# Performance work log

Hardware: AMD Instinct MI355X
Metric: run time of the kernel (lower is better)

Reference implementation:

```python
import jax, jax.numpy as jnp
import numpy as np

N = 50000          # nodes
E = 800000         # edges (avg degree 16)
IN_C = 3
HEADS = 4
NUM_GRAPHS = 8
NUM_CLASSES = 10


def setup_inputs() -> dict:
    key = jax.random.key(0)
    ks = jax.random.split(key, 12)
    x = jax.random.normal(ks[0], (N, IN_C), jnp.float32)
    edge_index = jax.random.randint(ks[1], (2, E), 0, N, dtype=jnp.int64)
    batch = jnp.sort(jax.random.randint(ks[2], (N,), 0, NUM_GRAPHS, dtype=jnp.int64))

    def glorot(k, shape, fan):
        return jax.random.normal(k, shape, jnp.float32) * np.float32(1.0 / np.sqrt(fan))

    return {
        "x": x, "edge_index": edge_index, "batch": batch,
        "fc0_w": glorot(ks[3], (IN_C, 16), IN_C), "fc0_b": jnp.zeros((16,), jnp.float32),
        "u1": glorot(ks[4], (16, HEADS), 16), "c1": jnp.zeros((HEADS,), jnp.float32),
        "w1": glorot(ks[5], (16, HEADS * 32), 16), "b1": jnp.zeros((32,), jnp.float32),
        "u2": glorot(ks[6], (32, HEADS), 32), "c2": jnp.zeros((HEADS,), jnp.float32),
        "w2": glorot(ks[7], (32, HEADS * 64), 32), "b2": jnp.zeros((64,), jnp.float32),
        "fc1_w": glorot(ks[8], (64, NUM_CLASSES), 64), "fc1_b": jnp.zeros((NUM_CLASSES,), jnp.float32),
    }


def feast_conv(x, src, dst, u, c, w, b, heads, out_c):
    """FeaStConv (t_inv=True): per-edge head softmax on (x_j - x_i), mean aggregation."""
    n = x.shape[0]
    # soft-assignment over heads: [E, H]
    q = jax.nn.softmax((x[src] - x[dst]) @ u + c, axis=-1)
    # transform at node level, then gather per edge: [E, H, out_c]
    xw = (x @ w).reshape(n, heads, out_c)
    msg = jnp.einsum('eh,ehc->ec', q, xw[src])           # [E, out_c]
    agg = jax.ops.segment_sum(msg, dst, num_segments=n)  # sum over incoming edges
    cnt = jax.ops.segment_sum(jnp.ones((src.shape[0],), x.dtype), dst, num_segments=n)
    return agg / jnp.maximum(cnt, 1.0)[:, None] + b


def global_mean_pool(x, batch, num_graphs):
    s = jax.ops.segment_sum(x, batch, num_segments=num_graphs)
    cnt = jax.ops.segment_sum(jnp.ones((x.shape[0],), x.dtype), batch, num_segments=num_graphs)
    return s / jnp.maximum(cnt, 1.0)[:, None]


def reference(x, edge_index, batch, fc0_w, fc0_b, u1, c1, w1, b1, u2, c2, w2, b2, fc1_w, fc1_b):
    src, dst = edge_index[0], edge_index[1]   # x_j = x[src], x_i = x[dst]
    h = jax.nn.relu(x @ fc0_w + fc0_b)                              # [N, 16]
    h = jax.nn.relu(feast_conv(h, src, dst, u1, c1, w1, b1, HEADS, 32))  # [N, 32]
    h = jax.nn.relu(feast_conv(h, src, dst, u2, c2, w2, b2, HEADS, 64))  # [N, 64]
    g = global_mean_pool(h, batch, NUM_GRAPHS)                      # [G, 64]
    # dropout is identity in eval mode
    return g @ fc1_w + fc1_b                                        # [G, num_classes]
```

## Files before the change

kernel.cpp:

```cpp
#include <hip/hip_runtime.h>

#define N_NODES 50000
#define N_EDGES 800000
#define HEADS 4
#define NUM_GRAPHS 8

#define EBLK ((N_EDGES + 255) / 256)
#define NBLK ((N_NODES + 255) / 256)

__global__ __launch_bounds__(256) void hist_fc0_kernel(
    const int* __restrict__ dst, int* __restrict__ deg, int* __restrict__ off,
    const float* __restrict__ x,
    const float* __restrict__ fc0_w, const float* __restrict__ fc0_b,
    const float* __restrict__ u1,
    float* __restrict__ h0, float* __restrict__ P1) {
  if (blockIdx.x < EBLK) {
    int e = blockIdx.x * 256 + threadIdx.x;
    if (e < N_EDGES) off[e] = atomicAdd(&deg[dst[e]], 1);
    return;
  }
  __shared__ float sW0[3 * 16];
  __shared__ float sB0[16];
  __shared__ float sU[16 * 4];
  for (int i = threadIdx.x; i < 48; i += 256) sW0[i] = fc0_w[i];
  for (int i = threadIdx.x; i < 16; i += 256) sB0[i] = fc0_b[i];
  for (int i = threadIdx.x; i < 64; i += 256) sU[i] = u1[i];
  __syncthreads();
  int n = (blockIdx.x - EBLK) * 256 + threadIdx.x;
  if (n >= N_NODES) return;
  float x0 = x[n * 3 + 0], x1 = x[n * 3 + 1], x2 = x[n * 3 + 2];
  float h[16];
#pragma unroll
  for (int j = 0; j < 16; j++) {
    float v = x0 * sW0[0 * 16 + j] + x1 * sW0[1 * 16 + j] + x2 * sW0[2 * 16 + j] + sB0[j];
    h[j] = fmaxf(v, 0.f);
    h0[(size_t)n * 16 + j] = h[j];
  }
  float p0 = 0.f, p1 = 0.f, p2 = 0.f, p3 = 0.f;
#pragma unroll
  for (int j = 0; j < 16; j++) {
    p0 += h[j] * sU[j * 4 + 0];
    p1 += h[j] * sU[j * 4 + 1];
    p2 += h[j] * sU[j * 4 + 2];
    p3 += h[j] * sU[j * 4 + 3];
  }
  reinterpret_cast<float4*>(P1)[n] = make_float4(p0, p1, p2, p3);
}

__global__ __launch_bounds__(256) void alloc_kernel(const int* __restrict__ deg,
                                                    int* __restrict__ gctr,
                                                    int* __restrict__ rowstart) {
  int i = blockIdx.x * blockDim.x + threadIdx.x;
  int lane = threadIdx.x & 63;
  int d = (i < N_NODES) ? deg[i] : 0;
  int pre = d;
#pragma unroll
  for (int offd = 1; offd < 64; offd <<= 1) {
    int v = __shfl_up(pre, offd, 64);
    if (lane >= offd) pre += v;
  }
  int total = __shfl(pre, 63, 64);
  int base = 0;
  if (lane == 63) base = atomicAdd(gctr, total);
  base = __shfl(base, 63, 64);
  if (i < N_NODES) rowstart[i] = base + pre - d;
}

__global__ __launch_bounds__(256) void scatter_kernel(const int* __restrict__ src,
                                                      const int* __restrict__ dst,
                                                      const int* __restrict__ rowstart,
                                                      const int* __restrict__ off,
                                                      int* __restrict__ src_perm) {
  int e = blockIdx.x * blockDim.x + threadIdx.x;
  if (e >= N_EDGES) return;
  src_perm[rowstart[dst[e]] + off[e]] = src[e];
}

__device__ __forceinline__ float4 edge_q(float4 Ps, float b0, float b1, float b2, float b3) {
  float l0 = Ps.x + b0, l1 = Ps.y + b1, l2 = Ps.z + b2, l3 = Ps.w + b3;
  float m = fmaxf(fmaxf(l0, l1), fmaxf(l2, l3));
  float e0 = __expf(l0 - m), e1 = __expf(l1 - m), e2 = __expf(l2 - m), e3 = __expf(l3 - m);
  float inv = 1.f / (e0 + e1 + e2 + e3);
  return make_float4(e0 * inv, e1 * inv, e2 * inv, e3 * inv);
}

__global__ __launch_bounds__(256) void agg1_kernel(
    const int* __restrict__ rowstart, const int* __restrict__ deg,
    const int* __restrict__ src_perm,
    const float* __restrict__ P1, const float* __restrict__ c1,
    const float* __restrict__ h0,
    float* __restrict__ A) {
  int wave = threadIdx.x >> 6;
  int lane = threadIdx.x & 63;
  int g = lane >> 4;
  int j = lane & 15;
  int node = blockIdx.x * 4 + wave;
  if (node >= N_NODES) return;
  float4 Pd = reinterpret_cast<const float4*>(P1)[node];
  float b0 = c1[0] - Pd.x, b1 = c1[1] - Pd.y, b2 = c1[2] - Pd.z, b3 = c1[3] - Pd.w;
  int e0 = rowstart[node];
  int e1 = e0 + deg[node];
  const float4* P4 = reinterpret_cast<const float4*>(P1);
  float a0 = 0.f, a1 = 0.f, a2 = 0.f, a3 = 0.f;
  int p = e0;
  for (; p + 16 <= e1; p += 16) {
    int sA = src_perm[p + 0 + g];
    int sB = src_perm[p + 4 + g];
    int sC = src_perm[p + 8 + g];
    int sD = src_perm[p + 12 + g];
    float4 PA = P4[sA];
    float4 PB = P4[sB];
    float4 PC = P4[sC];
    float4 PD = P4[sD];
    float fA = h0[(size_t)sA * 16 + j];
    float fB = h0[(size_t)sB * 16 + j];
    float fC = h0[(size_t)sC * 16 + j];
    float fD = h0[(size_t)sD * 16 + j];
    float4 qA = edge_q(PA, b0, b1, b2, b3);
    float4 qB = edge_q(PB, b0, b1, b2, b3);
    float4 qC = edge_q(PC, b0, b1, b2, b3);
    float4 qD = edge_q(PD, b0, b1, b2, b3);
    a0 += qA.x * fA + qB.x * fB + qC.x * fC + qD.x * fD;
    a1 += qA.y * fA + qB.y * fB + qC.y * fC + qD.y * fD;
    a2 += qA.z * fA + qB.z * fB + qC.z * fC + qD.z * fD;
    a3 += qA.w * fA + qB.w * fB + qC.w * fC + qD.w * fD;
  }
  for (; p + 4 <= e1; p += 4) {
    int s = src_perm[p + g];
    float4 Ps = P4[s];
    float f = h0[(size_t)s * 16 + j];
    float4 q = edge_q(Ps, b0, b1, b2, b3);
    a0 += q.x * f; a1 += q.y * f; a2 += q.z * f; a3 += q.w * f;
  }
  int rem = e1 - p;
  if (g < rem) {
    int s = src_perm[p + g];
    float4 Ps = P4[s];
    float f = h0[(size_t)s * 16 + j];
    float4 q = edge_q(Ps, b0, b1, b2, b3);
    a0 += q.x * f; a1 += q.y * f; a2 += q.z * f; a3 += q.w * f;
  }
  a0 += __shfl_xor(a0, 16, 64); a0 += __shfl_xor(a0, 32, 64);
  a1 += __shfl_xor(a1, 16, 64); a1 += __shfl_xor(a1, 32, 64);
  a2 += __shfl_xor(a2, 16, 64); a2 += __shfl_xor(a2, 32, 64);
  a3 += __shfl_xor(a3, 16, 64); a3 += __shfl_xor(a3, 32, 64);
  float o = (g == 0) ? a0 : (g == 1) ? a1 : (g == 2) ? a2 : a3;
  A[(size_t)node * 64 + lane] = o;
}

__global__ __launch_bounds__(256) void agg2_kernel(
    const int* __restrict__ rowstart, const int* __restrict__ deg,
    const int* __restrict__ src_perm,
    const float* __restrict__ P2, const float* __restrict__ c2,
    const float* __restrict__ h1,
    float* __restrict__ A) {
  int wave = threadIdx.x >> 6;
  int lane = threadIdx.x & 63;
  int g = lane >> 5;
  int j = lane & 31;
  int node = blockIdx.x * 4 + wave;
  if (node >= N_NODES) return;
  float4 Pd = reinterpret_cast<const float4*>(P2)[node];
  float b0 = c2[0] - Pd.x, b1 = c2[1] - Pd.y, b2 = c2[2] - Pd.z, b3 = c2[3] - Pd.w;
  int e0 = rowstart[node];
  int e1 = e0 + deg[node];
  const float4* P4 = reinterpret_cast<const float4*>(P2);
  float a0 = 0.f, a1 = 0.f, a2 = 0.f, a3 = 0.f;
  int p = e0;
  for (; p + 8 <= e1; p += 8) {
    int sA = src_perm[p + 0 + g];
    int sB = src_perm[p + 2 + g];
    int sC = src_perm[p + 4 + g];
    int sD = src_perm[p + 6 + g];
    float4 PA = P4[sA];
    float4 PB = P4[sB];
    float4 PC = P4[sC];
    float4 PD = P4[sD];
    float fA = h1[(size_t)sA * 32 + j];
    float fB = h1[(size_t)sB * 32 + j];
    float fC = h1[(size_t)sC * 32 + j];
    float fD = h1[(size_t)sD * 32 + j];
    float4 qA = edge_q(PA, b0, b1, b2, b3);
    float4 qB = edge_q(PB, b0, b1, b2, b3);
    float4 qC = edge_q(PC, b0, b1, b2, b3);
    float4 qD = edge_q(PD, b0, b1, b2, b3);
    a0 += qA.x * fA + qB.x * fB + qC.x * fC + qD.x * fD;
    a1 += qA.y * fA + qB.y * fB + qC.y * fC + qD.y * fD;
    a2 += qA.z * fA + qB.z * fB + qC.z * fC + qD.z * fD;
    a3 += qA.w * fA + qB.w * fB + qC.w * fC + qD.w * fD;
  }
  for (; p + 2 <= e1; p += 2) {
    int s = src_perm[p + g];
    float4 Ps = P4[s];
    float f = h1[(size_t)s * 32 + j];
    float4 q = edge_q(Ps, b0, b1, b2, b3);
    a0 += q.x * f; a1 += q.y * f; a2 += q.z * f; a3 += q.w * f;
  }
  int rem = e1 - p;
  if (g < rem) {
    int s = src_perm[p + g];
    float4 Ps = P4[s];
    float f = h1[(size_t)s * 32 + j];
    float4 q = edge_q(Ps, b0, b1, b2, b3);
    a0 += q.x * f; a1 += q.y * f; a2 += q.z * f; a3 += q.w * f;
  }
  a0 += __shfl_xor(a0, 32, 64);
  a1 += __shfl_xor(a1, 32, 64);
  a2 += __shfl_xor(a2, 32, 64);
  a3 += __shfl_xor(a3, 32, 64);
  float oa = (g == 0) ? a0 : a1;
  float ob = (g == 0) ? a2 : a3;
  A[(size_t)node * 128 + lane] = oa;
  A[(size_t)node * 128 + 64 + lane] = ob;
}

__global__ __launch_bounds__(256) void gemm1_kernel(
    const int* __restrict__ deg, const float* __restrict__ A,
    const float* __restrict__ w1, const float* __restrict__ b1,
    const float* __restrict__ u2,
    float* __restrict__ h1, float* __restrict__ P2) {
  __shared__ float sB[64 * 32];
  __shared__ float sU[32 * 4];
  for (int i = threadIdx.x; i < 64 * 32; i += 256) {
    int hj = i / 32, c = i % 32;
    sB[i] = w1[(hj % 16) * 128 + (hj / 16) * 32 + c];
  }
  for (int i = threadIdx.x; i < 128; i += 256) sU[i] = u2[i];
  __syncthreads();
  const float4* sB4 = reinterpret_cast<const float4*>(sB);
  int c4 = threadIdx.x & 7;
  int g = threadIdx.x >> 3;
  int n0 = blockIdx.x * 64 + g * 2;
  int n1 = n0 + 1;
  int na = min(n0, N_NODES - 1);
  int nb = min(n1, N_NODES - 1);
  const float4* A0 = reinterpret_cast<const float4*>(A + (size_t)na * 64);
  const float4* A1 = reinterpret_cast<const float4*>(A + (size_t)nb * 64);
  float4 bc = reinterpret_cast<const float4*>(b1)[c4];
  float4 acc0 = {0, 0, 0, 0}, acc1 = {0, 0, 0, 0};
#pragma unroll 2
  for (int k4 = 0; k4 < 16; k4++) {
    float4 a0 = A0[k4];
    float4 a1 = A1[k4];
    float4 w0 = sB4[(4 * k4 + 0) * 8 + c4];
    float4 wv1 = sB4[(4 * k4 + 1) * 8 + c4];
    float4 w2v = sB4[(4 * k4 + 2) * 8 + c4];
    float4 w3 = sB4[(4 * k4 + 3) * 8 + c4];
    acc0.x += a0.x * w0.x + a0.y * wv1.x + a0.z * w2v.x + a0.w * w3.x;
    acc0.y += a0.x * w0.y + a0.y * wv1.y + a0.z * w2v.y + a0.w * w3.y;
    acc0.z += a0.x * w0.z + a0.y * wv1.z + a0.z * w2v.z + a0.w * w3.z;
    acc0.w += a0.x * w0.w + a0.y * wv1.w + a0.z * w2v.w + a0.w * w3.w;
    acc1.x += a1.x * w0.x + a1.y * wv1.x + a1.z * w2v.x + a1.w * w3.x;
    acc1.y += a1.x * w0.y + a1.y * wv1.y + a1.z * w2v.y + a1.w * w3.y;
    acc1.z += a1.x * w0.z + a1.y * wv1.z + a1.z * w2v.z + a1.w * w3.z;
    acc1.w += a1.x * w0.w + a1.y * wv1.w + a1.z * w2v.w + a1.w * w3.w;
  }
  float inv0 = 1.f / fmaxf((float)deg[na], 1.f);
  float inv1 = 1.f / fmaxf((float)deg[nb], 1.f);
  float4 o0 = {fmaxf(acc0.x * inv0 + bc.x, 0.f), fmaxf(acc0.y * inv0 + bc.y, 0.f),
               fmaxf(acc0.z * inv0 + bc.z, 0.f), fmaxf(acc0.w * inv0 + bc.w, 0.f)};
  float4 o1 = {fmaxf(acc1.x * inv1 + bc.x, 0.f), fmaxf(acc1.y * inv1 + bc.y, 0.f),
               fmaxf(acc1.z * inv1 + bc.z, 0.f), fmaxf(acc1.w * inv1 + bc.w, 0.f)};
  if (n0 < N_NODES) reinterpret_cast<float4*>(h1 + (size_t)n0 * 32)[c4] = o0;
  if (n1 < N_NODES) reinterpret_cast<float4*>(h1 + (size_t)n1 * 32)[c4] = o1;
  float pa[4] = {0, 0, 0, 0}, pb[4] = {0, 0, 0, 0};
#pragma unroll
  for (int k = 0; k < 4; k++) {
    int c = 4 * c4 + k;
    float v0 = k == 0 ? o0.x : k == 1 ? o0.y : k == 2 ? o0.z : o0.w;
    float v1 = k == 0 ? o1.x : k == 1 ? o1.y : k == 2 ? o1.z : o1.w;
#pragma unroll
    for (int hh = 0; hh < 4; hh++) {
      pa[hh] += v0 * sU[c * 4 + hh];
      pb[hh] += v1 * sU[c * 4 + hh];
    }
  }
#pragma unroll
  for (int msk = 1; msk <= 4; msk <<= 1) {
#pragma unroll
    for (int hh = 0; hh < 4; hh++) {
      pa[hh] += __shfl_xor(pa[hh], msk, 64);
      pb[hh] += __shfl_xor(pb[hh], msk, 64);
    }
  }
  if (c4 == 0) {
    if (n0 < N_NODES)
      reinterpret_cast<float4*>(P2)[n0] = make_float4(pa[0], pa[1], pa[2], pa[3]);
    if (n1 < N_NODES)
      reinterpret_cast<float4*>(P2)[n1] = make_float4(pb[0], pb[1], pb[2], pb[3]);
  }
}

__global__ __launch_bounds__(256) void gemm2_kernel(
    const int* __restrict__ deg, const float* __restrict__ A,
    const float* __restrict__ w2, const float* __restrict__ b2,
    float* __restrict__ h2) {
  __shared__ float sB[128 * 64];
  for (int i = threadIdx.x; i < 128 * 64; i += 256) {
    int hj = i / 64, c = i % 64;
    sB[i] = w2[(hj % 32) * 256 + (hj / 32) * 64 + c];
  }
  __syncthreads();
  const float4* sB4 = reinterpret_cast<const float4*>(sB);
  int c4 = threadIdx.x & 15;
  int g = threadIdx.x >> 4;
  int n0 = blockIdx.x * 32 + g * 2;
  int n1 = n0 + 1;
  int na = min(n0, N_NODES - 1);
  int nb = min(n1, N_NODES - 1);
  const float4* A0 = reinterpret_cast<const float4*>(A + (size_t)na * 128);
  const float4* A1 = reinterpret_cast<const float4*>(A + (size_t)nb * 128);
  float4 bc = reinterpret_cast<const float4*>(b2)[c4];
  float4 acc0 = {0, 0, 0, 0}, acc1 = {0, 0, 0, 0};
#pragma unroll 2
  for (int k4 = 0; k4 < 32; k4++) {
    float4 a0 = A0[k4];
    float4 a1 = A1[k4];
    float4 w0 = sB4[(4 * k4 + 0) * 16 + c4];
    float4 wv1 = sB4[(4 * k4 + 1) * 16 + c4];
    float4 w2v = sB4[(4 * k4 + 2) * 16 + c4];
    float4 w3 = sB4[(4 * k4 + 3) * 16 + c4];
    acc0.x += a0.x * w0.x + a0.y * wv1.x + a0.z * w2v.x + a0.w * w3.x;
    acc0.y += a0.x * w0.y + a0.y * wv1.y + a0.z * w2v.y + a0.w * w3.y;
    acc0.z += a0.x * w0.z + a0.y * wv1.z + a0.z * w2v.z + a0.w * w3.z;
    acc0.w += a0.x * w0.w + a0.y * wv1.w + a0.z * w2v.w + a0.w * w3.w;
    acc1.x += a1.x * w0.x + a1.y * wv1.x + a1.z * w2v.x + a1.w * w3.x;
    acc1.y += a1.x * w0.y + a1.y * wv1.y + a1.z * w2v.y + a1.w * w3.y;
    acc1.z += a1.x * w0.z + a1.y * wv1.z + a1.z * w2v.z + a1.w * w3.z;
    acc1.w += a1.x * w0.w + a1.y * wv1.w + a1.z * w2v.w + a1.w * w3.w;
  }
  if (n0 < N_NODES) {
    float inv = 1.f / fmaxf((float)deg[n0], 1.f);
    float4 o = {fmaxf(acc0.x * inv + bc.x, 0.f), fmaxf(acc0.y * inv + bc.y, 0.f),
                fmaxf(acc0.z * inv + bc.z, 0.f), fmaxf(acc0.w * inv + bc.w, 0.f)};
    reinterpret_cast<float4*>(h2 + (size_t)n0 * 64)[c4] = o;
  }
  if (n1 < N_NODES) {
    float inv = 1.f / fmaxf((float)deg[n1], 1.f);
    float4 o = {fmaxf(acc1.x * inv + bc.x, 0.f), fmaxf(acc1.y * inv + bc.y, 0.f),
                fmaxf(acc1.z * inv + bc.z, 0.f), fmaxf(acc1.w * inv + bc.w, 0.f)};
    reinterpret_cast<float4*>(h2 + (size_t)n1 * 64)[c4] = o;
  }
}

#define POOL_CHUNK 64
__global__ __launch_bounds__(256) void pool_kernel(
    const float* __restrict__ h2, const int* __restrict__ batch,
    float* __restrict__ gsum, float* __restrict__ gcnt) {
  int grp = threadIdx.x / 64;
  int c = threadIdx.x % 64;
  int n0 = (blockIdx.x * 4 + grp) * POOL_CHUNK;
  int n1 = min(n0 + POOL_CHUNK, N_NODES);
  if (n0 >= N_NODES) return;
  float acc = 0.f;
  float cacc = 0.f;
  int curg = batch[n0];
  for (int n = n0; n < n1; n++) {
    int g = batch[n];
    float v = h2[(size_t)n * 64 + c];
    if (g != curg) {
      atomicAdd(&gsum[curg * 64 + c], acc);
      if (c == 0) atomicAdd(&gcnt[curg], cacc);
      acc = 0.f;
      cacc = 0.f;
      curg = g;
    }
    acc += v;
    cacc += 1.f;
  }
  atomicAdd(&gsum[curg * 64 + c], acc);
  if (c == 0) atomicAdd(&gcnt[curg], cacc);
}

__global__ __launch_bounds__(128) void head_kernel(
    const float* __restrict__ gsum, const float* __restrict__ gcnt,
    const float* __restrict__ fc1_w, const float* __restrict__ fc1_b,
    float* __restrict__ out) {
  int t = threadIdx.x;
  if (t >= NUM_GRAPHS * 10) return;
  int g = t / 10, k = t % 10;
  float inv = 1.f / fmaxf(gcnt[g], 1.f);
  float s = fc1_b[k];
#pragma unroll
  for (int c = 0; c < 64; c++) s += gsum[g * 64 + c] * inv * fc1_w[c * 10 + k];
  out[g * 10 + k] = s;
}

extern "C" void kernel_launch(void* const* d_in, const int* in_sizes, int n_in,
                              void* d_out, int out_size, void* d_ws, size_t ws_size,
                              hipStream_t stream) {
  const float* x = (const float*)d_in[0];
  const int* edge_index = (const int*)d_in[1];
  const int* batch = (const int*)d_in[2];
  const float* fc0_w = (const float*)d_in[3];
  const float* fc0_b = (const float*)d_in[4];
  const float* u1 = (const float*)d_in[5];
  const float* c1 = (const float*)d_in[6];
  const float* w1 = (const float*)d_in[7];
  const float* b1 = (const float*)d_in[8];
  const float* u2 = (const float*)d_in[9];
  const float* c2 = (const float*)d_in[10];
  const float* w2 = (const float*)d_in[11];
  const float* b2 = (const float*)d_in[12];
  const float* fc1_w = (const float*)d_in[13];
  const float* fc1_b = (const float*)d_in[14];
  float* out = (float*)d_out;

  const int* src = edge_index;
  const int* dst = edge_index + N_EDGES;

  char* wsb = (char*)d_ws;
  int* deg = (int*)wsb;
  int* gctr = deg + N_NODES;
  float* gsum = (float*)wsb + 50004;
  float* gcnt = gsum + NUM_GRAPHS * 64;
  int* rowstart = (int*)wsb + 50524;
  int* off = rowstart + N_NODES;
  int* src_perm = off + N_EDGES;
  float* h0 = (float*)wsb + 1700524;
  float* h1 = h0 + (size_t)N_NODES * 16;
  float* h2 = h1 + (size_t)N_NODES * 32;
  float* A = h2 + (size_t)N_NODES * 64;
  float* P1 = A + (size_t)N_NODES * 128;
  float* P2 = P1 + (size_t)N_NODES * 4;

  hipMemsetAsync(d_ws, 0, 50524 * sizeof(int), stream);

  int nblk = NBLK;
  int eblk = EBLK;
  int wblk = (N_NODES + 3) / 4;

  hist_fc0_kernel<<<eblk + nblk, 256, 0, stream>>>(dst, deg, off, x, fc0_w, fc0_b, u1, h0, P1);
  alloc_kernel<<<nblk, 256, 0, stream>>>(deg, gctr, rowstart);
  scatter_kernel<<<eblk, 256, 0, stream>>>(src, dst, rowstart, off, src_perm);

  agg1_kernel<<<wblk, 256, 0, stream>>>(rowstart, deg, src_perm, P1, c1, h0, A);
  gemm1_kernel<<<(N_NODES + 63) / 64, 256, 0, stream>>>(deg, A, w1, b1, u2, h1, P2);

  agg2_kernel<<<wblk, 256, 0, stream>>>(rowstart, deg, src_perm, P2, c2, h1, A);
  gemm2_kernel<<<(N_NODES + 31) / 32, 256, 0, stream>>>(deg, A, w2, b2, h2);

  int pblk = (N_NODES + POOL_CHUNK * 4 - 1) / (POOL_CHUNK * 4);
  pool_kernel<<<pblk, 256, 0, stream>>>(h2, batch, gsum, gcnt);
  head_kernel<<<1, 128, 0, stream>>>(gsum, gcnt, fc1_w, fc1_b, out);
}
```

Measured before the change: 275.3 us.

## Fuse all pipeline stages into one persistent cooperative kernel with grid syncs

Replaces the memset plus nine separate kernel launches with a single cooperative persistent kernel that runs histogram, scan, scatter, both aggregation and GEMM stages, pooling and the head in sequence, separated by grid-wide syncs. Each stage becomes a grid-stride loop over nodes, edges or tiles. The goal is to remove per-launch overhead and the gaps between kernels. In exchange there are about nine grid barriers, occupancy drops because of the 32 KB shared buffer, and some host API calls for occupancy queries are added on each launch.

```diff
diff --git a/kernel.cpp b/kernel.cpp
--- a/kernel.cpp
+++ b/kernel.cpp
@@ -1,80 +1,29 @@
 #include <hip/hip_runtime.h>
+#include <hip/hip_cooperative_groups.h>
+
+namespace cg = cooperative_groups;
 
 #define N_NODES 50000
 #define N_EDGES 800000
 #define HEADS 4
 #define NUM_GRAPHS 8
-
-#define EBLK ((N_EDGES + 255) / 256)
-#define NBLK ((N_NODES + 255) / 256)
-
-__global__ __launch_bounds__(256) void hist_fc0_kernel(
-    const int* __restrict__ dst, int* __restrict__ deg, int* __restrict__ off,
-    const float* __restrict__ x,
-    const float* __restrict__ fc0_w, const float* __restrict__ fc0_b,
-    const float* __restrict__ u1,
-    float* __restrict__ h0, float* __restrict__ P1) {
-  if (blockIdx.x < EBLK) {
-    int e = blockIdx.x * 256 + threadIdx.x;
-    if (e < N_EDGES) off[e] = atomicAdd(&deg[dst[e]], 1);
-    return;
-  }
-  __shared__ float sW0[3 * 16];
-  __shared__ float sB0[16];
-  __shared__ float sU[16 * 4];
-  for (int i = threadIdx.x; i < 48; i += 256) sW0[i] = fc0_w[i];
-  for (int i = threadIdx.x; i < 16; i += 256) sB0[i] = fc0_b[i];
-  for (int i = threadIdx.x; i < 64; i += 256) sU[i] = u1[i];
-  __syncthreads();
-  int n = (blockIdx.x - EBLK) * 256 + threadIdx.x;
-  if (n >= N_NODES) return;
-  float x0 = x[n * 3 + 0], x1 = x[n * 3 + 1], x2 = x[n * 3 + 2];
-  float h[16];
-#pragma unroll
-  for (int j = 0; j < 16; j++) {
-    float v = x0 * sW0[0 * 16 + j] + x1 * sW0[1 * 16 + j] + x2 * sW0[2 * 16 + j] + sB0[j];
-    h[j] = fmaxf(v, 0.f);
-    h0[(size_t)n * 16 + j] = h[j];
-  }
-  float p0 = 0.f, p1 = 0.f, p2 = 0.f, p3 = 0.f;
-#pragma unroll
-  for (int j = 0; j < 16; j++) {
-    p0 += h[j] * sU[j * 4 + 0];
-    p1 += h[j] * sU[j * 4 + 1];
-    p2 += h[j] * sU[j * 4 + 2];
-    p3 += h[j] * sU[j * 4 + 3];
-  }
-  reinterpret_cast<float4*>(P1)[n] = make_float4(p0, p1, p2, p3);
-}
-
-__global__ __launch_bounds__(256) void alloc_kernel(const int* __restrict__ deg,
-                                                    int* __restrict__ gctr,
-                                                    int* __restrict__ rowstart) {
-  int i = blockIdx.x * blockDim.x + threadIdx.x;
-  int lane = threadIdx.x & 63;
-  int d = (i < N_NODES) ? deg[i] : 0;
-  int pre = d;
-#pragma unroll
-  for (int offd = 1; offd < 64; offd <<= 1) {
-    int v = __shfl_up(pre, offd, 64);
-    if (lane >= offd) pre += v;
-  }
-  int total = __shfl(pre, 63, 64);
-  int base = 0;
-  if (lane == 63) base = atomicAdd(gctr, total);
-  base = __shfl(base, 63, 64);
-  if (i < N_NODES) rowstart[i] = base + pre - d;
-}
-
-__global__ __launch_bounds__(256) void scatter_kernel(const int* __restrict__ src,
-                                                      const int* __restrict__ dst,
-                                                      const int* __restrict__ rowstart,
-                                                      const int* __restrict__ off,
-                                                      int* __restrict__ src_perm) {
-  int e = blockIdx.x * blockDim.x + threadIdx.x;
-  if (e >= N_EDGES) return;
-  src_perm[rowstart[dst[e]] + off[e]] = src[e];
-}
+#define ZERO_WORDS 50524
+
+struct MegaArgs {
+  const int* src;
+  const int* dst;
+  const int* batch;
+  const float *x, *fc0_w, *fc0_b, *u1, *c1, *w1, *b1, *u2, *c2, *w2, *b2, *fc1_w, *fc1_b;
+  float* out;
+  int* deg;
+  int* gctr;
+  float* gsum;
+  float* gcnt;
+  int* rowstart;
+  int* off;
+  int* src_perm;
+  float *h0, *h1, *h2, *A, *P1, *P2;
+};
 
 __device__ __forceinline__ float4 edge_q(float4 Ps, float b0, float b1, float b2, float b3) {
   float l0 = Ps.x + b0, l1 = Ps.y + b1, l2 = Ps.z + b2, l3 = Ps.w + b3;
@@ -84,363 +33,413 @@
   return make_float4(e0 * inv, e1 * inv, e2 * inv, e3 * inv);
 }
 
-__global__ __launch_bounds__(256) void agg1_kernel(
-    const int* __restrict__ rowstart, const int* __restrict__ deg,
-    const int* __restrict__ src_perm,
-    const float* __restrict__ P1, const float* __restrict__ c1,
-    const float* __restrict__ h0,
-    float* __restrict__ A) {
-  int wave = threadIdx.x >> 6;
-  int lane = threadIdx.x & 63;
-  int g = lane >> 4;
-  int j = lane & 15;
-  int node = blockIdx.x * 4 + wave;
-  if (node >= N_NODES) return;
-  float4 Pd = reinterpret_cast<const float4*>(P1)[node];
-  float b0 = c1[0] - Pd.x, b1 = c1[1] - Pd.y, b2 = c1[2] - Pd.z, b3 = c1[3] - Pd.w;
-  int e0 = rowstart[node];
-  int e1 = e0 + deg[node];
-  const float4* P4 = reinterpret_cast<const float4*>(P1);
-  float a0 = 0.f, a1 = 0.f, a2 = 0.f, a3 = 0.f;
-  int p = e0;
-  for (; p + 16 <= e1; p += 16) {
-    int sA = src_perm[p + 0 + g];
-    int sB = src_perm[p + 4 + g];
-    int sC = src_perm[p + 8 + g];
-    int sD = src_perm[p + 12 + g];
-    float4 PA = P4[sA];
-    float4 PB = P4[sB];
-    float4 PC = P4[sC];
-    float4 PD = P4[sD];
-    float fA = h0[(size_t)sA * 16 + j];
-    float fB = h0[(size_t)sB * 16 + j];
-    float fC = h0[(size_t)sC * 16 + j];
-    float fD = h0[(size_t)sD * 16 + j];
-    float4 qA = edge_q(PA, b0, b1, b2, b3);
-    float4 qB = edge_q(PB, b0, b1, b2, b3);
-    float4 qC = edge_q(PC, b0, b1, b2, b3);
-    float4 qD = edge_q(PD, b0, b1, b2, b3);
-    a0 += qA.x * fA + qB.x * fB + qC.x * fC + qD.x * fD;
-    a1 += qA.y * fA + qB.y * fB + qC.y * fC + qD.y * fD;
-    a2 += qA.z * fA + qB.z * fB + qC.z * fC + qD.z * fD;
-    a3 += qA.w * fA + qB.w * fB + qC.w * fC + qD.w * fD;
-  }
-  for (; p + 4 <= e1; p += 4) {
-    int s = src_perm[p + g];
-    float4 Ps = P4[s];
-    float f = h0[(size_t)s * 16 + j];
-    float4 q = edge_q(Ps, b0, b1, b2, b3);
-    a0 += q.x * f; a1 += q.y * f; a2 += q.z * f; a3 += q.w * f;
-  }
-  int rem = e1 - p;
-  if (g < rem) {
-    int s = src_perm[p + g];
-    float4 Ps = P4[s];
-    float f = h0[(size_t)s * 16 + j];
-    float4 q = edge_q(Ps, b0, b1, b2, b3);
-    a0 += q.x * f; a1 += q.y * f; a2 += q.z * f; a3 += q.w * f;
-  }
-  a0 += __shfl_xor(a0, 16, 64); a0 += __shfl_xor(a0, 32, 64);
-  a1 += __shfl_xor(a1, 16, 64); a1 += __shfl_xor(a1, 32, 64);
-  a2 += __shfl_xor(a2, 16, 64); a2 += __shfl_xor(a2, 32, 64);
-  a3 += __shfl_xor(a3, 16, 64); a3 += __shfl_xor(a3, 32, 64);
-  float o = (g == 0) ? a0 : (g == 1) ? a1 : (g == 2) ? a2 : a3;
-  A[(size_t)node * 64 + lane] = o;
-}
-
-__global__ __launch_bounds__(256) void agg2_kernel(
-    const int* __restrict__ rowstart, const int* __restrict__ deg,
-    const int* __restrict__ src_perm,
-    const float* __restrict__ P2, const float* __restrict__ c2,
-    const float* __restrict__ h1,
-    float* __restrict__ A) {
-  int wave = threadIdx.x >> 6;
-  int lane = threadIdx.x & 63;
-  int g = lane >> 5;
-  int j = lane & 31;
-  int node = blockIdx.x * 4 + wave;
-  if (node >= N_NODES) return;
-  float4 Pd = reinterpret_cast<const float4*>(P2)[node];
-  float b0 = c2[0] - Pd.x, b1 = c2[1] - Pd.y, b2 = c2[2] - Pd.z, b3 = c2[3] - Pd.w;
-  int e0 = rowstart[node];
-  int e1 = e0 + deg[node];
-  const float4* P4 = reinterpret_cast<const float4*>(P2);
-  float a0 = 0.f, a1 = 0.f, a2 = 0.f, a3 = 0.f;
-  int p = e0;
-  for (; p + 8 <= e1; p += 8) {
-    int sA = src_perm[p + 0 + g];
-    int sB = src_perm[p + 2 + g];
-    int sC = src_perm[p + 4 + g];
-    int sD = src_perm[p + 6 + g];
-    float4 PA = P4[sA];
-    float4 PB = P4[sB];
-    float4 PC = P4[sC];
-    float4 PD = P4[sD];
-    float fA = h1[(size_t)sA * 32 + j];
-    float fB = h1[(size_t)sB * 32 + j];
-    float fC = h1[(size_t)sC * 32 + j];
-    float fD = h1[(size_t)sD * 32 + j];
-    float4 qA = edge_q(PA, b0, b1, b2, b3);
-    float4 qB = edge_q(PB, b0, b1, b2, b3);
-    float4 qC = edge_q(PC, b0, b1, b2, b3);
-    float4 qD = edge_q(PD, b0, b1, b2, b3);
-    a0 += qA.x * fA + qB.x * fB + qC.x * fC + qD.x * fD;
-    a1 += qA.y * fA + qB.y * fB + qC.y * fC + qD.y * fD;
-    a2 += qA.z * fA + qB.z * fB + qC.z * fC + qD.z * fD;
-    a3 += qA.w * fA + qB.w * fB + qC.w * fC + qD.w * fD;
-  }
-  for (; p + 2 <= e1; p += 2) {
-    int s = src_perm[p + g];
-    float4 Ps = P4[s];
-    float f = h1[(size_t)s * 32 + j];
-    float4 q = edge_q(Ps, b0, b1, b2, b3);
-    a0 += q.x * f; a1 += q.y * f; a2 += q.z * f; a3 += q.w * f;
-  }
-  int rem = e1 - p;
-  if (g < rem) {
-    int s = src_perm[p + g];
-    float4 Ps = P4[s];
-    float f = h1[(size_t)s * 32 + j];
-    float4 q = edge_q(Ps, b0, b1, b2, b3);
-    a0 += q.x * f; a1 += q.y * f; a2 += q.z * f; a3 += q.w * f;
-  }
-  a0 += __shfl_xor(a0, 32, 64);
-  a1 += __shfl_xor(a1, 32, 64);
-  a2 += __shfl_xor(a2, 32, 64);
-  a3 += __shfl_xor(a3, 32, 64);
-  float oa = (g == 0) ? a0 : a1;
-  float ob = (g == 0) ? a2 : a3;
-  A[(size_t)node * 128 + lane] = oa;
-  A[(size_t)node * 128 + 64 + lane] = ob;
-}
-
-__global__ __launch_bounds__(256) void gemm1_kernel(
-    const int* __restrict__ deg, const float* __restrict__ A,
-    const float* __restrict__ w1, const float* __restrict__ b1,
-    const float* __restrict__ u2,
-    float* __restrict__ h1, float* __restrict__ P2) {
-  __shared__ float sB[64 * 32];
-  __shared__ float sU[32 * 4];
-  for (int i = threadIdx.x; i < 64 * 32; i += 256) {
+__global__ __launch_bounds__(256) void mega_kernel(MegaArgs a) {
+  cg::grid_group grid = cg::this_grid();
+  const int tid = blockIdx.x * 256 + threadIdx.x;
+  const int nthreads = gridDim.x * 256;
+  const int gwave = tid >> 6;
+  const int nwaves = nthreads >> 6;
+  const int lane = threadIdx.x & 63;
+
+  __shared__ float sB[8192];
+
+  {
+    int* zero = a.deg;
+    for (int i = tid; i < ZERO_WORDS; i += nthreads) zero[i] = 0;
+  }
+  __threadfence();
+  grid.sync();
+
+  for (int i = threadIdx.x; i < 48; i += 256) sB[i] = a.fc0_w[i];
+  for (int i = threadIdx.x; i < 16; i += 256) sB[48 + i] = a.fc0_b[i];
+  for (int i = threadIdx.x; i < 64; i += 256) sB[64 + i] = a.u1[i];
+  __syncthreads();
+  for (int e = tid; e < N_EDGES; e += nthreads)
+    a.off[e] = atomicAdd(&a.deg[a.dst[e]], 1);
+  for (int n = tid; n < N_NODES; n += nthreads) {
+    float x0 = a.x[n * 3 + 0], x1 = a.x[n * 3 + 1], x2 = a.x[n * 3 + 2];
+    float h[16];
+#pragma unroll
+    for (int j = 0; j < 16; j++) {
+      float v = x0 * sB[j] + x1 * sB[16 + j] + x2 * sB[32 + j] + sB[48 + j];
+      h[j] = fmaxf(v, 0.f);
+      a.h0[(size_t)n * 16 + j] = h[j];
+    }
+    float p0 = 0.f, p1 = 0.f, p2 = 0.f, p3 = 0.f;
+#pragma unroll
+    for (int j = 0; j < 16; j++) {
+      p0 += h[j] * sB[64 + j * 4 + 0];
+      p1 += h[j] * sB[64 + j * 4 + 1];
+      p2 += h[j] * sB[64 + j * 4 + 2];
+      p3 += h[j] * sB[64 + j * 4 + 3];
+    }
+    reinterpret_cast<float4*>(a.P1)[n] = make_float4(p0, p1, p2, p3);
+  }
+  __threadfence();
+  grid.sync();
+
+  for (int base = 0; base < N_NODES; base += nthreads) {
+    int i = base + tid;
+    int d = (i < N_NODES) ? a.deg[i] : 0;
+    int pre = d;
+#pragma unroll
+    for (int o = 1; o < 64; o <<= 1) {
+      int v = __shfl_up(pre, o, 64);
+      if (lane >= o) pre += v;
+    }
+    int total = __shfl(pre, 63, 64);
+    int b = 0;
+    if (lane == 63) b = atomicAdd(a.gctr, total);
+    b = __shfl(b, 63, 64);
+    if (i < N_NODES) a.rowstart[i] = b + pre - d;
+  }
+  __threadfence();
+  grid.sync();
+
+  for (int e = tid; e < N_EDGES; e += nthreads)
+    a.src_perm[a.rowstart[a.dst[e]] + a.off[e]] = a.src[e];
+  __threadfence();
+  grid.sync();
+
+  {
+    const float4* P4 = reinterpret_cast<const float4*>(a.P1);
+    int g = lane >> 4;
+    int j = lane & 15;
+    float cb0 = a.c1[0], cb1 = a.c1[1], cb2 = a.c1[2], cb3 = a.c1[3];
+    for (int node = gwave; node < N_NODES; node += nwaves) {
+      float4 Pd = P4[node];
+      float b0 = cb0 - Pd.x, b1 = cb1 - Pd.y, b2 = cb2 - Pd.z, b3 = cb3 - Pd.w;
+      int e0 = a.rowstart[node];
+      int e1 = e0 + a.deg[node];
+      float a0 = 0.f, a1 = 0.f, a2 = 0.f, a3 = 0.f;
+      int p = e0;
+      for (; p + 16 <= e1; p += 16) {
+        int sA = a.src_perm[p + 0 + g];
+        int sBn = a.src_perm[p + 4 + g];
+        int sC = a.src_perm[p + 8 + g];
+        int sD = a.src_perm[p + 12 + g];
+        float4 PA = P4[sA];
+        float4 PB = P4[sBn];
+        float4 PC = P4[sC];
+        float4 PD = P4[sD];
+        float fA = a.h0[(size_t)sA * 16 + j];
+        float fB = a.h0[(size_t)sBn * 16 + j];
+        float fC = a.h0[(size_t)sC * 16 + j];
+        float fD = a.h0[(size_t)sD * 16 + j];
+        float4 qA = edge_q(PA, b0, b1, b2, b3);
+        float4 qB = edge_q(PB, b0, b1, b2, b3);
+        float4 qC = edge_q(PC, b0, b1, b2, b3);
+        float4 qD = edge_q(PD, b0, b1, b2, b3);
+        a0 += qA.x * fA + qB.x * fB + qC.x * fC + qD.x * fD;
+        a1 += qA.y * fA + qB.y * fB + qC.y * fC + qD.y * fD;
+        a2 += qA.z * fA + qB.z * fB + qC.z * fC + qD.z * fD;
+        a3 += qA.w * fA + qB.w * fB + qC.w * fC + qD.w * fD;
+      }
+      for (; p + 4 <= e1; p += 4) {
+        int s = a.src_perm[p + g];
+        float4 Ps = P4[s];
+        float f = a.h0[(size_t)s * 16 + j];
+        float4 q = edge_q(Ps, b0, b1, b2, b3);
+        a0 += q.x * f; a1 += q.y * f; a2 += q.z * f; a3 += q.w * f;
+      }
+      int rem = e1 - p;
+      if (g < rem) {
+        int s = a.src_perm[p + g];
+        float4 Ps = P4[s];
+        float f = a.h0[(size_t)s * 16 + j];
+        float4 q = edge_q(Ps, b0, b1, b2, b3);
+        a0 += q.x * f; a1 += q.y * f; a2 += q.z * f; a3 += q.w * f;
+      }
+      a0 += __shfl_xor(a0, 16, 64); a0 += __shfl_xor(a0, 32, 64);
+      a1 += __shfl_xor(a1, 16, 64); a1 += __shfl_xor(a1, 32, 64);
+      a2 += __shfl_xor(a2, 16, 64); a2 += __shfl_xor(a2, 32, 64);
+      a3 += __shfl_xor(a3, 16, 64); a3 += __shfl_xor(a3, 32, 64);
+      float o = (g == 0) ? a0 : (g == 1) ? a1 : (g == 2) ? a2 : a3;
+      a.A[(size_t)node * 64 + lane] = o;
+    }
+  }
+  __threadfence();
+  grid.sync();
+
+  for (int i = threadIdx.x; i < 2048; i += 256) {
     int hj = i / 32, c = i % 32;
-    sB[i] = w1[(hj % 16) * 128 + (hj / 16) * 32 + c];
-  }
-  for (int i = threadIdx.x; i < 128; i += 256) sU[i] = u2[i];
+    sB[i] = a.w1[(hj % 16) * 128 + (hj / 16) * 32 + c];
+  }
+  for (int i = threadIdx.x; i < 128; i += 256) sB[2048 + i] = a.u2[i];
   __syncthreads();
-  const float4* sB4 = reinterpret_cast<const float4*>(sB);
-  int c4 = threadIdx.x & 7;
-  int g = threadIdx.x >> 3;
-  int n0 = blockIdx.x * 64 + g * 2;
-  int n1 = n0 + 1;
-  int na = min(n0, N_NODES - 1);
-  int nb = min(n1, N_NODES - 1);
-  const float4* A0 = reinterpret_cast<const float4*>(A + (size_t)na * 64);
-  const float4* A1 = reinterpret_cast<const float4*>(A + (size_t)nb * 64);
-  float4 bc = reinterpret_cast<const float4*>(b1)[c4];
-  float4 acc0 = {0, 0, 0, 0}, acc1 = {0, 0, 0, 0};
+  {
+    const float4* sB4 = reinterpret_cast<const float4*>(sB);
+    const float* sU = sB + 2048;
+    int c4 = threadIdx.x & 7;
+    int gg = threadIdx.x >> 3;
+    int ntiles = (N_NODES + 63) / 64;
+    for (int bt = blockIdx.x; bt < ntiles; bt += gridDim.x) {
+      int n0 = bt * 64 + gg * 2;
+      int n1 = n0 + 1;
+      int na = min(n0, N_NODES - 1);
+      int nb = min(n1, N_NODES - 1);
+      const float4* A0 = reinterpret_cast<const float4*>(a.A + (size_t)na * 64);
+      const float4* A1 = reinterpret_cast<const float4*>(a.A + (size_t)nb * 64);
+      float4 bc = reinterpret_cast<const float4*>(a.b1)[c4];
+      float4 acc0 = {0, 0, 0, 0}, acc1 = {0, 0, 0, 0};
 #pragma unroll 2
-  for (int k4 = 0; k4 < 16; k4++) {
-    float4 a0 = A0[k4];
-    float4 a1 = A1[k4];
-    float4 w0 = sB4[(4 * k4 + 0) * 8 + c4];
-    float4 wv1 = sB4[(4 * k4 + 1) * 8 + c4];
-    float4 w2v = sB4[(4 * k4 + 2) * 8 + c4];
-    float4 w3 = sB4[(4 * k4 + 3) * 8 + c4];
-    acc0.x += a0.x * w0.x + a0.y * wv1.x + a0.z * w2v.x + a0.w * w3.x;
-    acc0.y += a0.x * w0.y + a0.y * wv1.y + a0.z * w2v.y + a0.w * w3.y;
-    acc0.z += a0.x * w0.z + a0.y * wv1.z + a0.z * w2v.z + a0.w * w3.z;
-    acc0.w += a0.x * w0.w + a0.y * wv1.w + a0.z * w2v.w + a0.w * w3.w;
-    acc1.x += a1.x * w0.x + a1.y * wv1.x + a1.z * w2v.x + a1.w * w3.x;
-    acc1.y += a1.x * w0.y + a1.y * wv1.y + a1.z * w2v.y + a1.w * w3.y;
-    acc1.z += a1.x * w0.z + a1.y * wv1.z + a1.z * w2v.z + a1.w * w3.z;
-    acc1.w += a1.x * w0.w + a1.y * wv1.w + a1.z * w2v.w + a1.w * w3.w;
-  }
-  float inv0 = 1.f / fmaxf((float)deg[na], 1.f);
-  float inv1 = 1.f / fmaxf((float)deg[nb], 1.f);
-  float4 o0 = {fmaxf(acc0.x * inv0 + bc.x, 0.f), fmaxf(acc0.y * inv0 + bc.y, 0.f),
-               fmaxf(acc0.z * inv0 + bc.z, 0.f), fmaxf(acc0.w * inv0 + bc.w, 0.f)};
-  float4 o1 = {fmaxf(acc1.x * inv1 + bc.x, 0.f), fmaxf(acc1.y * inv1 + bc.y, 0.f),
-               fmaxf(acc1.z * inv1 + bc.z, 0.f), fmaxf(acc1.w * inv1 + bc.w, 0.f)};
-  if (n0 < N_NODES) reinterpret_cast<float4*>(h1 + (size_t)n0 * 32)[c4] = o0;
-  if (n1 < N_NODES) reinterpret_cast<float4*>(h1 + (size_t)n1 * 32)[c4] = o1;
-  float pa[4] = {0, 0, 0, 0}, pb[4] = {0, 0, 0, 0};
-#pragma unroll
-  for (int k = 0; k < 4; k++) {
-    int c = 4 * c4 + k;
-    float v0 = k == 0 ? o0.x : k == 1 ? o0.y : k == 2 ? o0.z : o0.w;
-    float v1 = k == 0 ? o1.x : k == 1 ? o1.y : k == 2 ? o1.z : o1.w;
-#pragma unroll
-    for (int hh = 0; hh < 4; hh++) {
-      pa[hh] += v0 * sU[c * 4 + hh];
-      pb[hh] += v1 * sU[c * 4 + hh];
-    }
-  }
-#pragma unroll
-  for (int msk = 1; msk <= 4; msk <<= 1) {
-#pragma unroll
-    for (int hh = 0; hh < 4; hh++) {
-      pa[hh] += __shfl_xor(pa[hh], msk, 64);
-      pb[hh] += __shfl_xor(pb[hh], msk, 64);
-    }
-  }
-  if (c4 == 0) {
-    if (n0 < N_NODES)
-      reinterpret_cast<float4*>(P2)[n0] = make_float4(pa[0], pa[1], pa[2], pa[3]);
-    if (n1 < N_NODES)
-      reinterpret_cast<float4*>(P2)[n1] = make_float4(pb[0], pb[1], pb[2], pb[3]);
-  }
-}
-
-__global__ __launch_bounds__(256) void gemm2_kernel(
-    const int* __restrict__ deg, const float* __restrict__ A,
-    const float* __restrict__ w2, const float* __restrict__ b2,
-    float* __restrict__ h2) {
-  __shared__ float sB[128 * 64];
-  for (int i = threadIdx.x; i < 128 * 64; i += 256) {
+      for (int k4 = 0; k4 < 16; k4++) {
+        float4 a0 = A0[k4];
+        float4 a1 = A1[k4];
+        float4 w0 = sB4[(4 * k4 + 0) * 8 + c4];
+        float4 wv1 = sB4[(4 * k4 + 1) * 8 + c4];
+        float4 w2v = sB4[(4 * k4 + 2) * 8 + c4];
+        float4 w3 = sB4[(4 * k4 + 3) * 8 + c4];
+        acc0.x += a0.x * w0.x + a0.y * wv1.x + a0.z * w2v.x + a0.w * w3.x;
+        acc0.y += a0.x * w0.y + a0.y * wv1.y + a0.z * w2v.y + a0.w * w3.y;
+        acc0.z += a0.x * w0.z + a0.y * wv1.z + a0.z * w2v.z + a0.w * w3.z;
+        acc0.w += a0.x * w0.w + a0.y * wv1.w + a0.z * w2v.w + a0.w * w3.w;
+        acc1.x += a1.x * w0.x + a1.y * wv1.x + a1.z * w2v.x + a1.w * w3.x;
+        acc1.y += a1.x * w0.y + a1.y * wv1.y + a1.z * w2v.y + a1.w * w3.y;
+        acc1.z += a1.x * w0.z + a1.y * wv1.z + a1.z * w2v.z + a1.w * w3.z;
+        acc1.w += a1.x * w0.w + a1.y * wv1.w + a1.z * w2v.w + a1.w * w3.w;
+      }
+      float inv0 = 1.f / fmaxf((float)a.deg[na], 1.f);
+      float inv1 = 1.f / fmaxf((float)a.deg[nb], 1.f);
+      float4 o0 = {fmaxf(acc0.x * inv0 + bc.x, 0.f), fmaxf(acc0.y * inv0 + bc.y, 0.f),
+                   fmaxf(acc0.z * inv0 + bc.z, 0.f), fmaxf(acc0.w * inv0 + bc.w, 0.f)};
+      float4 o1 = {fmaxf(acc1.x * inv1 + bc.x, 0.f), fmaxf(acc1.y * inv1 + bc.y, 0.f),
+                   fmaxf(acc1.z * inv1 + bc.z, 0.f), fmaxf(acc1.w * inv1 + bc.w, 0.f)};
+      if (n0 < N_NODES) reinterpret_cast<float4*>(a.h1 + (size_t)n0 * 32)[c4] = o0;
+      if (n1 < N_NODES) reinterpret_cast<float4*>(a.h1 + (size_t)n1 * 32)[c4] = o1;
+      float pa[4] = {0, 0, 0, 0}, pb[4] = {0, 0, 0, 0};
+#pragma unroll
+      for (int k = 0; k < 4; k++) {
+        int c = 4 * c4 + k;
+        float v0 = k == 0 ? o0.x : k == 1 ? o0.y : k == 2 ? o0.z : o0.w;
+        float v1 = k == 0 ? o1.x : k == 1 ? o1.y : k == 2 ? o1.z : o1.w;
+#pragma unroll
+        for (int hh = 0; hh < 4; hh++) {
+          pa[hh] += v0 * sU[c * 4 + hh];
+          pb[hh] += v1 * sU[c * 4 + hh];
+        }
+      }
+#pragma unroll
+      for (int msk = 1; msk <= 4; msk <<= 1) {
+#pragma unroll
+        for (int hh = 0; hh < 4; hh++) {
+          pa[hh] += __shfl_xor(pa[hh], msk, 64);
+          pb[hh] += __shfl_xor(pb[hh], msk, 64);
+        }
+      }
+      if (c4 == 0) {
+        if (n0 < N_NODES)
+          reinterpret_cast<float4*>(a.P2)[n0] = make_float4(pa[0], pa[1], pa[2], pa[3]);
+        if (n1 < N_NODES)
+          reinterpret_cast<float4*>(a.P2)[n1] = make_float4(pb[0], pb[1], pb[2], pb[3]);
+      }
+    }
+  }
+  __threadfence();
+  grid.sync();
+
+  {
+    const float4* P4 = reinterpret_cast<const float4*>(a.P2);
+    int g = lane >> 5;
+    int j = lane & 31;
+    float cb0 = a.c2[0], cb1 = a.c2[1], cb2 = a.c2[2], cb3 = a.c2[3];
+    for (int node = gwave; node < N_NODES; node += nwaves) {
+      float4 Pd = P4[node];
+      float b0 = cb0 - Pd.x, b1 = cb1 - Pd.y, b2 = cb2 - Pd.z, b3 = cb3 - Pd.w;
+      int e0 = a.rowstart[node];
+      int e1 = e0 + a.deg[node];
+      float a0 = 0.f, a1 = 0.f, a2 = 0.f, a3 = 0.f;
+      int p = e0;
+      for (; p + 8 <= e1; p += 8) {
+        int sA = a.src_perm[p + 0 + g];
+        int sBn = a.src_perm[p + 2 + g];
+        int sC = a.src_perm[p + 4 + g];
+        int sD = a.src_perm[p + 6 + g];
+        float4 PA = P4[sA];
+        float4 PB = P4[sBn];
+        float4 PC = P4[sC];
+        float4 PD = P4[sD];
+        float fA = a.h1[(size_t)sA * 32 + j];
+        float fB = a.h1[(size_t)sBn * 32 + j];
+        float fC = a.h1[(size_t)sC * 32 + j];
+        float fD = a.h1[(size_t)sD * 32 + j];
+        float4 qA = edge_q(PA, b0, b1, b2, b3);
+        float4 qB = edge_q(PB, b0, b1, b2, b3);
+        float4 qC = edge_q(PC, b0, b1, b2, b3);
+        float4 qD = edge_q(PD, b0, b1, b2, b3);
+        a0 += qA.x * fA + qB.x * fB + qC.x * fC + qD.x * fD;
+        a1 += qA.y * fA + qB.y * fB + qC.y * fC + qD.y * fD;
+        a2 += qA.z * fA + qB.z * fB + qC.z * fC + qD.z * fD;
+        a3 += qA.w * fA + qB.w * fB + qC.w * fC + qD.w * fD;
+      }
+      for (; p + 2 <= e1; p += 2) {
+        int s = a.src_perm[p + g];
+        float4 Ps = P4[s];
+        float f = a.h1[(size_t)s * 32 + j];
+        float4 q = edge_q(Ps, b0, b1, b2, b3);
+        a0 += q.x * f; a1 += q.y * f; a2 += q.z * f; a3 += q.w * f;
+      }
+      int rem = e1 - p;
+      if (g < rem) {
+        int s = a.src_perm[p + g];
+        float4 Ps = P4[s];
+        float f = a.h1[(size_t)s * 32 + j];
+        float4 q = edge_q(Ps, b0, b1, b2, b3);
+        a0 += q.x * f; a1 += q.y * f; a2 += q.z * f; a3 += q.w * f;
+      }
+      a0 += __shfl_xor(a0, 32, 64);
+      a1 += __shfl_xor(a1, 32, 64);
+      a2 += __shfl_xor(a2, 32, 64);
+      a3 += __shfl_xor(a3, 32, 64);
+      float oa = (g == 0) ? a0 : a1;
+      float ob = (g == 0) ? a2 : a3;
+      a.A[(size_t)node * 128 + lane] = oa;
+      a.A[(size_t)node * 128 + 64 + lane] = ob;
+    }
+  }
+  __threadfence();
+  grid.sync();
+
+  for (int i = threadIdx.x; i < 8192; i += 256) {
     int hj = i / 64, c = i % 64;
-    sB[i] = w2[(hj % 32) * 256 + (hj / 32) * 64 + c];
+    sB[i] = a.w2[(hj % 32) * 256 + (hj / 32) * 64 + c];
   }
   __syncthreads();
-  const float4* sB4 = reinterpret_cast<const float4*>(sB);
-  int c4 = threadIdx.x & 15;
-  int g = threadIdx.x >> 4;
-  int n0 = blockIdx.x * 32 + g * 2;
-  int n1 = n0 + 1;
-  int na = min(n0, N_NODES - 1);
-  int nb = min(n1, N_NODES - 1);
-  const float4* A0 = reinterpret_cast<const float4*>(A + (size_t)na * 128);
-  const float4* A1 = reinterpret_cast<const float4*>(A + (size_t)nb * 128);
-  float4 bc = reinterpret_cast<const float4*>(b2)[c4];
-  float4 acc0 = {0, 0, 0, 0}, acc1 = {0, 0, 0, 0};
+  {
+    const float4* sB4 = reinterpret_cast<const float4*>(sB);
+    int c4 = threadIdx.x & 15;
+    int gg = threadIdx.x >> 4;
+    int ntiles = (N_NODES + 31) / 32;
+    for (int bt = blockIdx.x; bt < ntiles; bt += gridDim.x) {
+      int n0 = bt * 32 + gg * 2;
+      int n1 = n0 + 1;
+      int na = min(n0, N_NODES - 1);
+      int nb = min(n1, N_NODES - 1);
+      const float4* A0 = reinterpret_cast<const float4*>(a.A + (size_t)na * 128);
+      const float4* A1 = reinterpret_cast<const float4*>(a.A + (size_t)nb * 128);
+      float4 bc = reinterpret_cast<const float4*>(a.b2)[c4];
+      float4 acc0 = {0, 0, 0, 0}, acc1 = {0, 0, 0, 0};
 #pragma unroll 2
-  for (int k4 = 0; k4 < 32; k4++) {
-    float4 a0 = A0[k4];
-    float4 a1 = A1[k4];
-    float4 w0 = sB4[(4 * k4 + 0) * 16 + c4];
-    float4 wv1 = sB4[(4 * k4 + 1) * 16 + c4];
-    float4 w2v = sB4[(4 * k4 + 2) * 16 + c4];
-    float4 w3 = sB4[(4 * k4 + 3) * 16 + c4];
-    acc0.x += a0.x * w0.x + a0.y * wv1.x + a0.z * w2v.x + a0.w * w3.x;
-    acc0.y += a0.x * w0.y + a0.y * wv1.y + a0.z * w2v.y + a0.w * w3.y;
-    acc0.z += a0.x * w0.z + a0.y * wv1.z + a0.z * w2v.z + a0.w * w3.z;
-    acc0.w += a0.x * w0.w + a0.y * wv1.w + a0.z * w2v.w + a0.w * w3.w;
-    acc1.x += a1.x * w0.x + a1.y * wv1.x + a1.z * w2v.x + a1.w * w3.x;
-    acc1.y += a1.x * w0.y + a1.y * wv1.y + a1.z * w2v.y + a1.w * w3.y;
-    acc1.z += a1.x * w0.z + a1.y * wv1.z + a1.z * w2v.z + a1.w * w3.z;
-    acc1.w += a1.x * w0.w + a1.y * wv1.w + a1.z * w2v.w + a1.w * w3.w;
-  }
-  if (n0 < N_NODES) {
-    float inv = 1.f / fmaxf((float)deg[n0], 1.f);
-    float4 o = {fmaxf(acc0.x * inv + bc.x, 0.f), fmaxf(acc0.y * inv + bc.y, 0.f),
-                fmaxf(acc0.z * inv + bc.z, 0.f), fmaxf(acc0.w * inv + bc.w, 0.f)};
-    reinterpret_cast<float4*>(h2 + (size_t)n0 * 64)[c4] = o;
-  }
-  if (n1 < N_NODES) {
-    float inv = 1.f / fmaxf((float)deg[n1], 1.f);
-    float4 o = {fmaxf(acc1.x * inv + bc.x, 0.f), fmaxf(acc1.y * inv + bc.y, 0.f),
-                fmaxf(acc1.z * inv + bc.z, 0.f), fmaxf(acc1.w * inv + bc.w, 0.f)};
-    reinterpret_cast<float4*>(h2 + (size_t)n1 * 64)[c4] = o;
-  }
-}
-
-#define POOL_CHUNK 64
-__global__ __launch_bounds__(256) void pool_kernel(
-    const float* __restrict__ h2, const int* __restrict__ batch,
-    float* __restrict__ gsum, float* __restrict__ gcnt) {
-  int grp = threadIdx.x / 64;
-  int c = threadIdx.x % 64;
-  int n0 = (blockIdx.x * 4 + grp) * POOL_CHUNK;
-  int n1 = min(n0 + POOL_CHUNK, N_NODES);
-  if (n0 >= N_NODES) return;
-  float acc = 0.f;
-  float cacc = 0.f;
-  int curg = batch[n0];
-  for (int n = n0; n < n1; n++) {
-    int g = batch[n];
-    float v = h2[(size_t)n * 64 + c];
-    if (g != curg) {
-      atomicAdd(&gsum[curg * 64 + c], acc);
-      if (c == 0) atomicAdd(&gcnt[curg], cacc);
-      acc = 0.f;
-      cacc = 0.f;
-      curg = g;
-    }
-    acc += v;
-    cacc += 1.f;
-  }
-  atomicAdd(&gsum[curg * 64 + c], acc);
-  if (c == 0) atomicAdd(&gcnt[curg], cacc);
-}
-
-__global__ __launch_bounds__(128) void head_kernel(
-    const float* __restrict__ gsum, const float* __restrict__ gcnt,
-    const float* __restrict__ fc1_w, const float* __restrict__ fc1_b,
-    float* __restrict__ out) {
-  int t = threadIdx.x;
-  if (t >= NUM_GRAPHS * 10) return;
-  int g = t / 10, k = t % 10;
-  float inv = 1.f / fmaxf(gcnt[g], 1.f);
-  float s = fc1_b[k];
-#pragma unroll
-  for (int c = 0; c < 64; c++) s += gsum[g * 64 + c] * inv * fc1_w[c * 10 + k];
-  out[g * 10 + k] = s;
+      for (int k4 = 0; k4 < 32; k4++) {
+        float4 a0 = A0[k4];
+        float4 a1 = A1[k4];
+        float4 w0 = sB4[(4 * k4 + 0) * 16 + c4];
+        float4 wv1 = sB4[(4 * k4 + 1) * 16 + c4];
+        float4 w2v = sB4[(4 * k4 + 2) * 16 + c4];
+        float4 w3 = sB4[(4 * k4 + 3) * 16 + c4];
+        acc0.x += a0.x * w0.x + a0.y * wv1.x + a0.z * w2v.x + a0.w * w3.x;
+        acc0.y += a0.x * w0.y + a0.y * wv1.y + a0.z * w2v.y + a0.w * w3.y;
+        acc0.z += a0.x * w0.z + a0.y * wv1.z + a0.z * w2v.z + a0.w * w3.z;
+        acc0.w += a0.x * w0.w + a0.y * wv1.w + a0.z * w2v.w + a0.w * w3.w;
+        acc1.x += a1.x * w0.x + a1.y * wv1.x + a1.z * w2v.x + a1.w * w3.x;
+        acc1.y += a1.x * w0.y + a1.y * wv1.y + a1.z * w2v.y + a1.w * w3.y;
+        acc1.z += a1.x * w0.z + a1.y * wv1.z + a1.z * w2v.z + a1.w * w3.z;
+        acc1.w += a1.x * w0.w + a1.y * wv1.w + a1.z * w2v.w + a1.w * w3.w;
+      }
+      if (n0 < N_NODES) {
+        float inv = 1.f / fmaxf((float)a.deg[n0], 1.f);
+        float4 o = {fmaxf(acc0.x * inv + bc.x, 0.f), fmaxf(acc0.y * inv + bc.y, 0.f),
+                    fmaxf(acc0.z * inv + bc.z, 0.f), fmaxf(acc0.w * inv + bc.w, 0.f)};
+        reinterpret_cast<float4*>(a.h2 + (size_t)n0 * 64)[c4] = o;
+      }
+      if (n1 < N_NODES) {
+        float inv = 1.f / fmaxf((float)a.deg[n1], 1.f);
+        float4 o = {fmaxf(acc1.x * inv + bc.x, 0.f), fmaxf(acc1.y * inv + bc.y, 0.f),
+                    fmaxf(acc1.z * inv + bc.z, 0.f), fmaxf(acc1.w * inv + bc.w, 0.f)};
+        reinterpret_cast<float4*>(a.h2 + (size_t)n1 * 64)[c4] = o;
+      }
+    }
+  }
+  __threadfence();
+  grid.sync();
+
+  {
+    int c = lane;
+    int nchunks = (N_NODES + 63) / 64;
+    for (int chunk = gwave; chunk < nchunks; chunk += nwaves) {
+      int n0 = chunk * 64;
+      int n1 = min(n0 + 64, N_NODES);
+      float acc = 0.f;
+      float cacc = 0.f;
+      int curg = a.batch[n0];
+      for (int n = n0; n < n1; n++) {
+        int g = a.batch[n];
+        float v = a.h2[(size_t)n * 64 + c];
+        if (g != curg) {
+          atomicAdd(&a.gsum[curg * 64 + c], acc);
+          if (c == 0) atomicAdd(&a.gcnt[curg], cacc);
+          acc = 0.f;
+          cacc = 0.f;
+          curg = g;
+        }
+        acc += v;
+        cacc += 1.f;
+      }
+      atomicAdd(&a.gsum[curg * 64 + c], acc);
+      if (c == 0) atomicAdd(&a.gcnt[curg], cacc);
+    }
+  }
+  __threadfence();
+  grid.sync();
+
+  if (blockIdx.x == 0 && threadIdx.x < NUM_GRAPHS * 10) {
+    int g = threadIdx.x / 10, k = threadIdx.x % 10;
+    float inv = 1.f / fmaxf(a.gcnt[g], 1.f);
+    float s = a.fc1_b[k];
+#pragma unroll
+    for (int c = 0; c < 64; c++) s += a.gsum[g * 64 + c] * inv * a.fc1_w[c * 10 + k];
+    a.out[g * 10 + k] = s;
+  }
 }
 
 extern "C" void kernel_launch(void* const* d_in, const int* in_sizes, int n_in,
                               void* d_out, int out_size, void* d_ws, size_t ws_size,
                               hipStream_t stream) {
-  const float* x = (const float*)d_in[0];
+  MegaArgs a;
+  a.x = (const float*)d_in[0];
   const int* edge_index = (const int*)d_in[1];
-  const int* batch = (const int*)d_in[2];
-  const float* fc0_w = (const float*)d_in[3];
-  const float* fc0_b = (const float*)d_in[4];
-  const float* u1 = (const float*)d_in[5];
-  const float* c1 = (const float*)d_in[6];
-  const float* w1 = (const float*)d_in[7];
-  const float* b1 = (const float*)d_in[8];
-  const float* u2 = (const float*)d_in[9];
-  const float* c2 = (const float*)d_in[10];
-  const float* w2 = (const float*)d_in[11];
-  const float* b2 = (const float*)d_in[12];
-  const float* fc1_w = (const float*)d_in[13];
-  const float* fc1_b = (const float*)d_in[14];
-  float* out = (float*)d_out;
-
-  const int* src = edge_index;
-  const int* dst = edge_index + N_EDGES;
+  a.batch = (const int*)d_in[2];
+  a.fc0_w = (const float*)d_in[3];
+  a.fc0_b = (const float*)d_in[4];
+  a.u1 = (const float*)d_in[5];
+  a.c1 = (const float*)d_in[6];
+  a.w1 = (const float*)d_in[7];
+  a.b1 = (const float*)d_in[8];
+  a.u2 = (const float*)d_in[9];
+  a.c2 = (const float*)d_in[10];
+  a.w2 = (const float*)d_in[11];
+  a.b2 = (const float*)d_in[12];
+  a.fc1_w = (const float*)d_in[13];
+  a.fc1_b = (const float*)d_in[14];
+  a.out = (float*)d_out;
+  a.src = edge_index;
+  a.dst = edge_index + N_EDGES;
 
   char* wsb = (char*)d_ws;
-  int* deg = (int*)wsb;
-  int* gctr = deg + N_NODES;
-  float* gsum = (float*)wsb + 50004;
-  float* gcnt = gsum + NUM_GRAPHS * 64;
-  int* rowstart = (int*)wsb + 50524;
-  int* off = rowstart + N_NODES;
-  int* src_perm = off + N_EDGES;
-  float* h0 = (float*)wsb + 1700524;
-  float* h1 = h0 + (size_t)N_NODES * 16;
-  float* h2 = h1 + (size_t)N_NODES * 32;
-  float* A = h2 + (size_t)N_NODES * 64;
-  float* P1 = A + (size_t)N_NODES * 128;
-  float* P2 = P1 + (size_t)N_NODES * 4;
-
-  hipMemsetAsync(d_ws, 0, 50524 * sizeof(int), stream);
-
-  int nblk = NBLK;
-  int eblk = EBLK;
-  int wblk = (N_NODES + 3) / 4;
-
-  hist_fc0_kernel<<<eblk + nblk, 256, 0, stream>>>(dst, deg, off, x, fc0_w, fc0_b, u1, h0, P1);
-  alloc_kernel<<<nblk, 256, 0, stream>>>(deg, gctr, rowstart);
-  scatter_kernel<<<eblk, 256, 0, stream>>>(src, dst, rowstart, off, src_perm);
-
-  agg1_kernel<<<wblk, 256, 0, stream>>>(rowstart, deg, src_perm, P1, c1, h0, A);
-  gemm1_kernel<<<(N_NODES + 63) / 64, 256, 0, stream>>>(deg, A, w1, b1, u2, h1, P2);
-
-  agg2_kernel<<<wblk, 256, 0, stream>>>(rowstart, deg, src_perm, P2, c2, h1, A);
-  gemm2_kernel<<<(N_NODES + 31) / 32, 256, 0, stream>>>(deg, A, w2, b2, h2);
-
-  int pblk = (N_NODES + POOL_CHUNK * 4 - 1) / (POOL_CHUNK * 4);
-  pool_kernel<<<pblk, 256, 0, stream>>>(h2, batch, gsum, gcnt);
-  head_kernel<<<1, 128, 0, stream>>>(gsum, gcnt, fc1_w, fc1_b, out);
+  a.deg = (int*)wsb;
+  a.gctr = a.deg + N_NODES;
+  a.gsum = (float*)wsb + 50004;
+  a.gcnt = a.gsum + NUM_GRAPHS * 64;
+  a.rowstart = (int*)wsb + 50524;
+  a.off = a.rowstart + N_NODES;
+  a.src_perm = a.off + N_EDGES;
+  a.h0 = (float*)wsb + 1700524;
+  a.h1 = a.h0 + (size_t)N_NODES * 16;
+  a.h2 = a.h1 + (size_t)N_NODES * 32;
+  a.A = a.h2 + (size_t)N_NODES * 64;
+  a.P1 = a.A + (size_t)N_NODES * 128;
+  a.P2 = a.P1 + (size_t)N_NODES * 4;
+
+  int dev = 0;
+  hipGetDevice(&dev);
+  int numCU = 0;
+  hipDeviceGetAttribute(&numCU, hipDeviceAttributeMultiprocessorCount, dev);
+  int blocksPerCU = 0;
+  hipOccupancyMaxActiveBlocksPerMultiprocessor(&blocksPerCU, (const void*)mega_kernel, 256, 0);
+  if (numCU <= 0) numCU = 256;
+  if (blocksPerCU <= 0) blocksPerCU = 1;
+  int G = numCU * blocksPerCU;
+
+  void* args[] = {(void*)&a};
+  hipLaunchCooperativeKernel((const void*)mega_kernel, dim3(G), dim3(256), args, 0, stream);
 }
```

Result: slower. 951.7 us (+245.8%).
